# Kernel optimization log

Measured on AMD Instinct MI355X. Metric: run time of the kernel, lower is better.

## Reference

```python
import jax, jax.numpy as jnp
import numpy as np
from jax import lax

B, NUM_E, NUM_R, H, C, K = 8192, 20000, 500, 512, 50, 3
EPS = 1e-5


def batchnorm(x, g, b, axes, shape):
    # training-mode BN: biased batch statistics (matches torch default forward)
    m = jnp.mean(x, axis=axes, keepdims=True)
    v = jnp.var(x, axis=axes, keepdims=True)
    return (x - m) / jnp.sqrt(v + EPS) * g.reshape(shape) + b.reshape(shape)


def setup_inputs() -> dict:
    key = jax.random.key(0)
    ks = jax.random.split(key, 12)
    facts = jax.random.randint(ks[0], (B, 3), 0, NUM_R)
    ent_emb = jax.random.normal(ks[1], (NUM_E, H), jnp.float32)
    rel_emb = jax.random.normal(ks[2], (NUM_R, H), jnp.float32)
    e_r_bias = jax.random.normal(ks[3], (NUM_E, H), jnp.float32)
    conv_w = jax.random.normal(ks[4], (C, 3, K), jnp.float32) * (1.0 / np.sqrt(3 * K))
    conv_b = jnp.zeros((C,), jnp.float32)
    fc_w = jax.random.normal(ks[5], (H, H * C), jnp.float32) * (1.0 / np.sqrt(H * C))
    fc_b = jnp.zeros((H,), jnp.float32)
    bn0_g = jnp.ones((3,), jnp.float32); bn0_b = jnp.zeros((3,), jnp.float32)
    bn1_g = jnp.ones((C,), jnp.float32); bn1_b = jnp.zeros((C,), jnp.float32)
    bn2_g = jnp.ones((H,), jnp.float32); bn2_b = jnp.zeros((H,), jnp.float32)
    return {"facts": facts, "ent_emb": ent_emb, "rel_emb": rel_emb, "e_r_bias": e_r_bias,
            "conv_w": conv_w, "conv_b": conv_b, "fc_w": fc_w, "fc_b": fc_b,
            "bn0_g": bn0_g, "bn0_b": bn0_b, "bn1_g": bn1_g, "bn1_b": bn1_b,
            "bn2_g": bn2_g, "bn2_b": bn2_b}


def reference(facts, ent_emb, rel_emb, e_r_bias, conv_w, conv_b, fc_w, fc_b,
              bn0_g, bn0_b, bn1_g, bn1_b, bn2_g, bn2_b):
    e_s = ent_emb[facts[:, 0]]        # (B, H)
    e_r = rel_emb[facts[:, 1]]        # (B, H)
    bias = e_r_bias[facts[:, 0]]      # (B, H)
    x = jnp.stack([e_s, e_r, bias], axis=1)            # (B, 3, H)
    x = batchnorm(x, bn0_g, bn0_b, (0, 2), (1, 3, 1))  # BatchNorm1d(3)
    pad = K // 2
    x = lax.conv_general_dilated(x, conv_w, window_strides=(1,),
                                 padding=((pad, pad),),
                                 dimension_numbers=("NCH", "OIH", "NCH"))
    x = x + conv_b[None, :, None]                      # (B, C, H)
    x = batchnorm(x, bn1_g, bn1_b, (0, 2), (1, C, 1))  # BatchNorm1d(C)
    x = jax.nn.relu(x)
    x = x.reshape(B, C * H)
    x = x @ fc_w.T + fc_b                              # (B, H)
    x = batchnorm(x, bn2_g, bn2_b, (0,), (1, H))       # BatchNorm1d(H), len>1
    x = jax.nn.relu(x)
    score = x @ ent_emb.T                              # (B, NUM_E)
    # F.softmax then log == log_softmax
    return jax.nn.log_softmax(score, axis=-1)
```

## Files before the change

kernel.cpp:

```cpp
#include <hip/hip_runtime.h>

#define B_SZ   8192
#define NUM_E  20000
#define H_DIM  512
#define C_DIM  50
#define KHW    25600
#define EPS    1e-5f
#define KSPLIT 8

typedef short bf16x8 __attribute__((ext_vector_type(8)));
typedef float f32x4  __attribute__((ext_vector_type(4)));

__device__ __forceinline__ float bf2f(unsigned short u) {
  return __uint_as_float(((unsigned int)u) << 16);
}
__device__ __forceinline__ unsigned short f2bf(float f) {
  unsigned int u = __float_as_uint(f);
  return (unsigned short)((u + 0x7FFFu + ((u >> 16) & 1u)) >> 16);
}

__global__ __launch_bounds__(256) void cvt_bf16_kernel(const float* __restrict__ in,
                                                       unsigned short* __restrict__ out,
                                                       int n4) {
  int i = blockIdx.x * 256 + threadIdx.x;
  int stride = gridDim.x * 256;
  for (; i < n4; i += stride) {
    float4 v = reinterpret_cast<const float4*>(in)[i];
    ushort4 o;
    o.x = f2bf(v.x); o.y = f2bf(v.y); o.z = f2bf(v.z); o.w = f2bf(v.w);
    reinterpret_cast<ushort4*>(out)[i] = o;
  }
}

__global__ __launch_bounds__(256) void bn0_stats_kernel(const int* __restrict__ facts,
                                                        const float* __restrict__ ent,
                                                        const float* __restrict__ rel,
                                                        const float* __restrict__ bias,
                                                        float* __restrict__ stats) {
  const int tid = threadIdx.x;
  float s0=0.f,s1=0.f,s2=0.f,q0=0.f,q1=0.f,q2=0.f;
  const int stride = gridDim.x * 256;
  for (int i = blockIdx.x * 256 + tid; i < B_SZ * H_DIM; i += stride) {
    int b = i >> 9, h = i & 511;
    int f0 = facts[b * 3 + 0], f1 = facts[b * 3 + 1];
    float v0 = ent[f0 * H_DIM + h];
    float v1 = rel[f1 * H_DIM + h];
    float v2 = bias[f0 * H_DIM + h];
    s0 += v0; q0 += v0 * v0;
    s1 += v1; q1 += v1 * v1;
    s2 += v2; q2 += v2 * v2;
  }
  __shared__ float red[256];
  float vals[6] = {s0, s1, s2, q0, q1, q2};
  for (int j = 0; j < 6; ++j) {
    red[tid] = vals[j]; __syncthreads();
    for (int off = 128; off > 0; off >>= 1) {
      if (tid < off) red[tid] += red[tid + off];
      __syncthreads();
    }
    if (tid == 0) atomicAdd(&stats[j], red[0]);
    __syncthreads();
  }
}

__global__ __launch_bounds__(256) void xn_kernel(const int* __restrict__ facts,
                                                 const float* __restrict__ ent,
                                                 const float* __restrict__ rel,
                                                 const float* __restrict__ bias,
                                                 const float* __restrict__ g0,
                                                 const float* __restrict__ b0,
                                                 const float* __restrict__ stats,
                                                 unsigned short* __restrict__ xn) {
  const float invN = 1.0f / 4194304.0f;
  float a[3], c[3];
  #pragma unroll
  for (int ch = 0; ch < 3; ++ch) {
    float mean = stats[ch] * invN;
    float var  = stats[3 + ch] * invN - mean * mean;
    float sc = g0[ch] * rsqrtf(var + EPS);
    a[ch] = sc;
    c[ch] = b0[ch] - mean * sc;
  }
  const int stride = gridDim.x * 256;
  for (int i = blockIdx.x * 256 + threadIdx.x; i < B_SZ * H_DIM; i += stride) {
    int b = i >> 9, h = i & 511;
    int f0 = facts[b * 3 + 0], f1 = facts[b * 3 + 1];
    xn[(b * 3 + 0) * H_DIM + h] = f2bf(fmaf(ent[f0 * H_DIM + h],  a[0], c[0]));
    xn[(b * 3 + 1) * H_DIM + h] = f2bf(fmaf(rel[f1 * H_DIM + h],  a[1], c[1]));
    xn[(b * 3 + 2) * H_DIM + h] = f2bf(fmaf(bias[f0 * H_DIM + h], a[2], c[2]));
  }
}

__global__ __launch_bounds__(256) void conv_stats_kernel(const unsigned short* __restrict__ xn,
                                                         const float* __restrict__ conv_w,
                                                         const float* __restrict__ conv_b,
                                                         float* __restrict__ stats) {
  const int tid = threadIdx.x;
  const int cg = blockIdx.y;
  float w[8][9], cb[8];
  #pragma unroll
  for (int j = 0; j < 8; ++j) {
    int c = cg * 8 + j;
    if (c < C_DIM) {
      #pragma unroll
      for (int t = 0; t < 9; ++t) w[j][t] = conv_w[c * 9 + t];
      cb[j] = conv_b[c];
    } else {
      #pragma unroll
      for (int t = 0; t < 9; ++t) w[j][t] = 0.f;
      cb[j] = 0.f;
    }
  }
  float s[8], qv[8];
  #pragma unroll
  for (int j = 0; j < 8; ++j) { s[j] = 0.f; qv[j] = 0.f; }
  const int stride = gridDim.x * 256;
  for (int i = blockIdx.x * 256 + tid; i < B_SZ * H_DIM; i += stride) {
    int b = i >> 9, h = i & 511;
    float xv[9];
    #pragma unroll
    for (int ii = 0; ii < 3; ++ii) {
      const unsigned short* row = xn + ((size_t)b * 3 + ii) * H_DIM;
      xv[ii * 3 + 0] = (h > 0)   ? bf2f(row[h - 1]) : 0.f;
      xv[ii * 3 + 1] = bf2f(row[h]);
      xv[ii * 3 + 2] = (h < 511) ? bf2f(row[h + 1]) : 0.f;
    }
    #pragma unroll
    for (int j = 0; j < 8; ++j) {
      float v = cb[j];
      #pragma unroll
      for (int t = 0; t < 9; ++t) v = fmaf(w[j][t], xv[t], v);
      s[j] += v; qv[j] += v * v;
    }
  }
  __shared__ float red[256];
  #pragma unroll 1
  for (int j = 0; j < 8; ++j) {
    int c = cg * 8 + j;
    red[tid] = s[j]; __syncthreads();
    for (int off = 128; off > 0; off >>= 1) {
      if (tid < off) red[tid] += red[tid + off];
      __syncthreads();
    }
    if (tid == 0 && c < C_DIM) atomicAdd(&stats[8 + c], red[0]);
    __syncthreads();
    red[tid] = qv[j]; __syncthreads();
    for (int off = 128; off > 0; off >>= 1) {
      if (tid < off) red[tid] += red[tid + off];
      __syncthreads();
    }
    if (tid == 0 && c < C_DIM) atomicAdd(&stats[64 + c], red[0]);
    __syncthreads();
  }
}

__global__ __launch_bounds__(64) void bn1_fold_kernel(const float* __restrict__ conv_w,
                                                      const float* __restrict__ conv_b,
                                                      const float* __restrict__ g1,
                                                      const float* __restrict__ b1,
                                                      const float* __restrict__ stats,
                                                      float* __restrict__ cwf) {
  const int c = threadIdx.x;
  if (c >= C_DIM) return;
  const float invN = 1.0f / 4194304.0f;
  float mean = stats[8 + c] * invN;
  float var  = stats[64 + c] * invN - mean * mean;
  float sc = g1[c] * rsqrtf(var + EPS);
  float tc = fmaf(sc, conv_b[c], b1[c] - mean * sc);
  #pragma unroll
  for (int t = 0; t < 9; ++t) cwf[c * 10 + t] = conv_w[c * 9 + t] * sc;
  cwf[c * 10 + 9] = tc;
}

__global__ __launch_bounds__(256) void fc_gemm_kernel(const unsigned short* __restrict__ xn,
                                                      const unsigned short* __restrict__ fcw,
                                                      const float* __restrict__ cwf,
                                                      float* __restrict__ z) {
  const int tid  = threadIdx.x;
  const int m0   = blockIdx.x * 128;
  const int n0   = blockIdx.y * 128;
  const int hs   = blockIdx.z * 64;
  const int lane = tid & 63;
  const int wave = tid >> 6;
  const int wm   = (wave >> 1) * 64;
  const int wn   = (wave & 1) * 64;
  const int l15  = lane & 15;
  const int qd   = lane >> 4;
  const int am   = tid >> 1;
  const int ah   = (tid & 1) * 16;

  __shared__ unsigned short xstage[128][3][36];
  __shared__ unsigned short albuf[2][128][40];

  f32x4 acc[4][4];
  #pragma unroll
  for (int a = 0; a < 4; ++a)
    #pragma unroll
    for (int b = 0; b < 4; ++b) {
      f32x4 zv = {0.f, 0.f, 0.f, 0.f};
      acc[a][b] = zv;
    }

  const unsigned short* bbase[4];
  #pragma unroll
  for (int tn = 0; tn < 4; ++tn)
    bbase[tn] = fcw + (size_t)(n0 + wn + tn * 16 + l15) * KHW + qd * 8;

  float xw[3][18];

  for (int h0 = hs; h0 < hs + 64; h0 += 32) {
    __syncthreads();
    for (int idx = tid; idx < 128 * 3 * 34; idx += 256) {
      int m = idx / 102;
      int rem = idx - m * 102;
      int i = rem / 34;
      int x = rem - i * 34;
      int h = h0 - 1 + x;
      unsigned short v = 0;
      if (h >= 0 && h < H_DIM) v = xn[((size_t)(m0 + m) * 3 + i) * H_DIM + h];
      xstage[m][i][x] = v;
    }
    __syncthreads();
    #pragma unroll
    for (int i = 0; i < 3; ++i) {
      const unsigned int* p = (const unsigned int*)&xstage[am][i][ah];
      #pragma unroll
      for (int j = 0; j < 9; ++j) {
        unsigned int u = p[j];
        xw[i][2 * j]     = __uint_as_float(u << 16);
        xw[i][2 * j + 1] = __uint_as_float(u & 0xFFFF0000u);
      }
    }

    auto agen = [&](int c, int bb) {
      float w[9], tc;
      const float* cw = cwf + c * 10;
      #pragma unroll
      for (int t = 0; t < 9; ++t) w[t] = cw[t];
      tc = cw[9];
      unsigned int pk[8];
      #pragma unroll
      for (int kp = 0; kp < 8; ++kp) {
        float vv[2];
        #pragma unroll
        for (int e = 0; e < 2; ++e) {
          int kk = kp * 2 + e;
          float v = tc;
          #pragma unroll
          for (int i = 0; i < 3; ++i) {
            v = fmaf(w[i * 3 + 0], xw[i][kk],     v);
            v = fmaf(w[i * 3 + 1], xw[i][kk + 1], v);
            v = fmaf(w[i * 3 + 2], xw[i][kk + 2], v);
          }
          vv[e] = fmaxf(v, 0.f);
        }
        asm("v_cvt_pk_bf16_f32 %0, %1, %2" : "=v"(pk[kp]) : "v"(vv[0]), "v"(vv[1]));
      }
      uint4* d = (uint4*)&albuf[bb][am][ah];
      d[0] = make_uint4(pk[0], pk[1], pk[2], pk[3]);
      d[1] = make_uint4(pk[4], pk[5], pk[6], pk[7]);
    };

    agen(0, 0);
    bf16x8 bcur[4];
    #pragma unroll
    for (int tn = 0; tn < 4; ++tn)
      bcur[tn] = *(const bf16x8*)(bbase[tn] + h0);
    __syncthreads();

    #pragma unroll 1
    for (int c = 0; c < C_DIM; ++c) {
      bf16x8 af[4];
      #pragma unroll
      for (int tm = 0; tm < 4; ++tm)
        af[tm] = *(const bf16x8*)&albuf[c & 1][wm + tm * 16 + l15][qd * 8];
      #pragma unroll
      for (int tm = 0; tm < 4; ++tm)
        #pragma unroll
        for (int tn = 0; tn < 4; ++tn)
          acc[tm][tn] = __builtin_amdgcn_mfma_f32_16x16x32_bf16(af[tm], bcur[tn], acc[tm][tn], 0, 0, 0);
      if (c + 1 < C_DIM) {
        bf16x8 bnew[4];
        #pragma unroll
        for (int tn = 0; tn < 4; ++tn)
          bnew[tn] = *(const bf16x8*)(bbase[tn] + (c + 1) * H_DIM + h0);
        agen(c + 1, (c + 1) & 1);
        __syncthreads();
        #pragma unroll
        for (int tn = 0; tn < 4; ++tn) bcur[tn] = bnew[tn];
      } else {
        __syncthreads();
      }
    }
  }

  #pragma unroll
  for (int tm = 0; tm < 4; ++tm)
    #pragma unroll
    for (int tn = 0; tn < 4; ++tn) {
      int col = n0 + wn + tn * 16 + l15;
      #pragma unroll
      for (int r = 0; r < 4; ++r) {
        int row = m0 + wm + tm * 16 + qd * 4 + r;
        atomicAdd(&z[(size_t)row * H_DIM + col], acc[tm][tn][r]);
      }
    }
}

__global__ __launch_bounds__(256) void bn2_stats_kernel(const float* __restrict__ z,
                                                        float* __restrict__ stats) {
  const int tid = threadIdx.x;
  const int col = blockIdx.y * 64 + (tid & 63);
  float s = 0.f, qq = 0.f;
  for (int r = blockIdx.x * 4 + (tid >> 6); r < B_SZ; r += gridDim.x * 4) {
    float v = z[(size_t)r * H_DIM + col];
    s += v; qq += v * v;
  }
  __shared__ float ls[256], lq[256];
  ls[tid] = s; lq[tid] = qq;
  __syncthreads();
  if (tid < 64) {
    s  = ls[tid] + ls[tid + 64] + ls[tid + 128] + ls[tid + 192];
    qq = lq[tid] + lq[tid + 64] + lq[tid + 128] + lq[tid + 192];
    atomicAdd(&stats[128 + col], s);
    atomicAdd(&stats[640 + col], qq);
  }
}

__global__ __launch_bounds__(256) void zr_kernel(const float* __restrict__ z,
                                                 const float* __restrict__ stats,
                                                 const float* __restrict__ g2,
                                                 const float* __restrict__ b2,
                                                 unsigned short* __restrict__ zrb) {
  const float invB = 1.0f / 8192.0f;
  const int stride = gridDim.x * 256;
  for (int i = blockIdx.x * 256 + threadIdx.x; i < B_SZ * H_DIM; i += stride) {
    int col = i & 511;
    float mean = stats[128 + col] * invB;
    float var  = stats[640 + col] * invB - mean * mean;
    float sc = g2[col] * rsqrtf(var + EPS);
    float tc = b2[col] - mean * sc;
    float v = fmaf(z[i], sc, tc);
    zrb[i] = f2bf(fmaxf(v, 0.f));
  }
}

__global__ __launch_bounds__(256) void score_gemm_kernel(const unsigned short* __restrict__ zrb,
                                                         const unsigned short* __restrict__ entb,
                                                         float* __restrict__ out) {
  const int tid  = threadIdx.x;
  const int m0   = blockIdx.x * 128;
  const int n0   = blockIdx.y * 128;
  const int lane = tid & 63;
  const int wave = tid >> 6;
  const int wm   = (wave >> 1) * 64;
  const int wn   = (wave & 1) * 64;
  const int l15  = lane & 15;
  const int qd   = lane >> 4;

  f32x4 acc[4][4];
  #pragma unroll
  for (int a = 0; a < 4; ++a)
    #pragma unroll
    for (int b = 0; b < 4; ++b) {
      f32x4 zv = {0.f, 0.f, 0.f, 0.f};
      acc[a][b] = zv;
    }

  const unsigned short* ap[4];
  const unsigned short* bp[4];
  #pragma unroll
  for (int t = 0; t < 4; ++t) {
    ap[t] = zrb + (size_t)(m0 + wm + t * 16 + l15) * H_DIM + qd * 8;
    int e = n0 + wn + t * 16 + l15;
    if (e >= NUM_E) e = NUM_E - 1;
    bp[t] = entb + (size_t)e * H_DIM + qd * 8;
  }
  #pragma unroll 2
  for (int k0 = 0; k0 < H_DIM; k0 += 32) {
    bf16x8 af[4], bf[4];
    #pragma unroll
    for (int t = 0; t < 4; ++t) {
      af[t] = *(const bf16x8*)(ap[t] + k0);
      bf[t] = *(const bf16x8*)(bp[t] + k0);
    }
    #pragma unroll
    for (int tm = 0; tm < 4; ++tm)
      #pragma unroll
      for (int tn = 0; tn < 4; ++tn)
        acc[tm][tn] = __builtin_amdgcn_mfma_f32_16x16x32_bf16(af[tm], bf[tn], acc[tm][tn], 0, 0, 0);
  }
  #pragma unroll
  for (int tm = 0; tm < 4; ++tm)
    #pragma unroll
    for (int tn = 0; tn < 4; ++tn) {
      int col = n0 + wn + tn * 16 + l15;
      if (col < NUM_E) {
        #pragma unroll
        for (int r = 0; r < 4; ++r) {
          int row = m0 + wm + tm * 16 + qd * 4 + r;
          out[(size_t)row * NUM_E + col] = acc[tm][tn][r];
        }
      }
    }
}

__global__ __launch_bounds__(256) void logsoftmax_kernel(float* __restrict__ out) {
  const int b = blockIdx.x;
  float* row = out + (size_t)b * NUM_E;
  const int tid = threadIdx.x;
  float m = -3.0e38f, s = 0.f;
  for (int c = tid; c < NUM_E; c += 256) {
    float x = row[c];
    if (x > m) { s = s * __expf(m - x) + 1.f; m = x; }
    else       { s += __expf(x - m); }
  }
  __shared__ float lm[256], ls[256];
  lm[tid] = m; ls[tid] = s;
  __syncthreads();
  for (int off = 128; off > 0; off >>= 1) {
    if (tid < off) {
      float m2 = lm[tid + off], s2 = ls[tid + off];
      float m1 = lm[tid],       s1 = ls[tid];
      float M = fmaxf(m1, m2);
      ls[tid] = s1 * __expf(m1 - M) + s2 * __expf(m2 - M);
      lm[tid] = M;
    }
    __syncthreads();
  }
  const float lse = lm[0] + __logf(ls[0]);
  for (int c = tid; c < NUM_E; c += 256) row[c] -= lse;
}

extern "C" void kernel_launch(void* const* d_in, const int* in_sizes, int n_in,
                              void* d_out, int out_size, void* d_ws, size_t ws_size,
                              hipStream_t stream) {
  const int*   facts  = (const int*)d_in[0];
  const float* ent    = (const float*)d_in[1];
  const float* rel    = (const float*)d_in[2];
  const float* erb    = (const float*)d_in[3];
  const float* conv_w = (const float*)d_in[4];
  const float* conv_b = (const float*)d_in[5];
  const float* fc_w   = (const float*)d_in[6];
  const float* g0     = (const float*)d_in[8];
  const float* b0     = (const float*)d_in[9];
  const float* g1     = (const float*)d_in[10];
  const float* b1     = (const float*)d_in[11];
  const float* g2     = (const float*)d_in[12];
  const float* b2     = (const float*)d_in[13];

  char* ws = (char*)d_ws;
  float*          stats = (float*)ws;
  float*          cwf   = (float*)(ws + 8192);
  unsigned short* xn    = (unsigned short*)(ws + 16384);
  unsigned short* fcw   = (unsigned short*)(ws + 25182208);
  unsigned short* entb  = (unsigned short*)(ws + 51396608);
  float*          z     = (float*)(ws + 71876608);
  unsigned short* zrb   = (unsigned short*)(ws + 88653824);
  float* out = (float*)d_out;

  hipMemsetAsync(stats, 0, 16384, stream);
  hipMemsetAsync(z, 0, 16777216, stream);
  cvt_bf16_kernel<<<2048, 256, 0, stream>>>(ent, entb, (NUM_E * H_DIM) / 4);
  cvt_bf16_kernel<<<2048, 256, 0, stream>>>(fc_w, fcw, (H_DIM * KHW) / 4);
  bn0_stats_kernel<<<1024, 256, 0, stream>>>(facts, ent, rel, erb, stats);
  xn_kernel<<<1024, 256, 0, stream>>>(facts, ent, rel, erb, g0, b0, stats, xn);
  conv_stats_kernel<<<dim3(512, 7), 256, 0, stream>>>(xn, conv_w, conv_b, stats);
  bn1_fold_kernel<<<1, 64, 0, stream>>>(conv_w, conv_b, g1, b1, stats, cwf);
  fc_gemm_kernel<<<dim3(64, 4, KSPLIT), 256, 0, stream>>>(xn, fcw, cwf, z);
  bn2_stats_kernel<<<dim3(64, 8), 256, 0, stream>>>(z, stats);
  zr_kernel<<<2048, 256, 0, stream>>>(z, stats, g2, b2, zrb);
  score_gemm_kernel<<<dim3(64, 157), 256, 0, stream>>>(zrb, entb, out);
  logsoftmax_kernel<<<8192, 256, 0, stream>>>(out);
}
```

Measured before the change: 2.682 ms.

## Fuse partial log-sum-exp into score GEMM and widen FC GEMM tiles to full N

The score GEMM epilogue now computes per-row, per-column-block max and sum-exp partials from its accumulators and writes them to workspace. A small kernel then reduces these into a per-row LSE, and a vectorized kernel subtracts it. This replaces the old logsoftmax pass, which read the output twice. Separately, the FC GEMM now uses 512-thread blocks that each cover all 512 output columns, so the conv-derived A tile is generated once per row block rather than four times, at the cost of more accumulator registers per thread.

```diff
diff --git a/kernel.cpp b/kernel.cpp
--- a/kernel.cpp
+++ b/kernel.cpp
@@ -7,6 +7,7 @@
 #define KHW    25600
 #define EPS    1e-5f
 #define KSPLIT 8
+#define NBLK   157
 
 typedef short bf16x8 __attribute__((ext_vector_type(8)));
 typedef float f32x4  __attribute__((ext_vector_type(4)));
@@ -172,45 +173,44 @@
   cwf[c * 10 + 9] = tc;
 }
 
-__global__ __launch_bounds__(256) void fc_gemm_kernel(const unsigned short* __restrict__ xn,
+__global__ __launch_bounds__(512) void fc_gemm_kernel(const unsigned short* __restrict__ xn,
                                                       const unsigned short* __restrict__ fcw,
                                                       const float* __restrict__ cwf,
                                                       float* __restrict__ z) {
   const int tid  = threadIdx.x;
   const int m0   = blockIdx.x * 128;
-  const int n0   = blockIdx.y * 128;
-  const int hs   = blockIdx.z * 64;
+  const int hs   = blockIdx.y * 64;
   const int lane = tid & 63;
   const int wave = tid >> 6;
-  const int wm   = (wave >> 1) * 64;
-  const int wn   = (wave & 1) * 64;
+  const int wm   = (wave >> 2) * 64;
+  const int wn   = (wave & 3) * 128;
   const int l15  = lane & 15;
   const int qd   = lane >> 4;
-  const int am   = tid >> 1;
-  const int ah   = (tid & 1) * 16;
+  const int am   = tid >> 2;
+  const int ah   = (tid & 3) * 8;
 
   __shared__ unsigned short xstage[128][3][36];
   __shared__ unsigned short albuf[2][128][40];
 
-  f32x4 acc[4][4];
+  f32x4 acc[4][8];
   #pragma unroll
   for (int a = 0; a < 4; ++a)
     #pragma unroll
-    for (int b = 0; b < 4; ++b) {
+    for (int b = 0; b < 8; ++b) {
       f32x4 zv = {0.f, 0.f, 0.f, 0.f};
       acc[a][b] = zv;
     }
 
-  const unsigned short* bbase[4];
-  #pragma unroll
-  for (int tn = 0; tn < 4; ++tn)
-    bbase[tn] = fcw + (size_t)(n0 + wn + tn * 16 + l15) * KHW + qd * 8;
-
-  float xw[3][18];
+  const unsigned short* bbase[8];
+  #pragma unroll
+  for (int tn = 0; tn < 8; ++tn)
+    bbase[tn] = fcw + (size_t)(wn + tn * 16 + l15) * KHW + qd * 8;
+
+  float xw[3][10];
 
   for (int h0 = hs; h0 < hs + 64; h0 += 32) {
     __syncthreads();
-    for (int idx = tid; idx < 128 * 3 * 34; idx += 256) {
+    for (int idx = tid; idx < 128 * 3 * 34; idx += 512) {
       int m = idx / 102;
       int rem = idx - m * 102;
       int i = rem / 34;
@@ -225,7 +225,7 @@
     for (int i = 0; i < 3; ++i) {
       const unsigned int* p = (const unsigned int*)&xstage[am][i][ah];
       #pragma unroll
-      for (int j = 0; j < 9; ++j) {
+      for (int j = 0; j < 5; ++j) {
         unsigned int u = p[j];
         xw[i][2 * j]     = __uint_as_float(u << 16);
         xw[i][2 * j + 1] = __uint_as_float(u & 0xFFFF0000u);
@@ -238,9 +238,9 @@
       #pragma unroll
       for (int t = 0; t < 9; ++t) w[t] = cw[t];
       tc = cw[9];
-      unsigned int pk[8];
-      #pragma unroll
-      for (int kp = 0; kp < 8; ++kp) {
+      unsigned int pk[4];
+      #pragma unroll
+      for (int kp = 0; kp < 4; ++kp) {
         float vv[2];
         #pragma unroll
         for (int e = 0; e < 2; ++e) {
@@ -256,15 +256,13 @@
         }
         asm("v_cvt_pk_bf16_f32 %0, %1, %2" : "=v"(pk[kp]) : "v"(vv[0]), "v"(vv[1]));
       }
-      uint4* d = (uint4*)&albuf[bb][am][ah];
-      d[0] = make_uint4(pk[0], pk[1], pk[2], pk[3]);
-      d[1] = make_uint4(pk[4], pk[5], pk[6], pk[7]);
+      *(uint4*)&albuf[bb][am][ah] = make_uint4(pk[0], pk[1], pk[2], pk[3]);
     };
 
     agen(0, 0);
-    bf16x8 bcur[4];
-    #pragma unroll
-    for (int tn = 0; tn < 4; ++tn)
+    bf16x8 bcur[8];
+    #pragma unroll
+    for (int tn = 0; tn < 8; ++tn)
       bcur[tn] = *(const bf16x8*)(bbase[tn] + h0);
     __syncthreads();
 
@@ -277,17 +275,17 @@
       #pragma unroll
       for (int tm = 0; tm < 4; ++tm)
         #pragma unroll
-        for (int tn = 0; tn < 4; ++tn)
+        for (int tn = 0; tn < 8; ++tn)
           acc[tm][tn] = __builtin_amdgcn_mfma_f32_16x16x32_bf16(af[tm], bcur[tn], acc[tm][tn], 0, 0, 0);
       if (c + 1 < C_DIM) {
-        bf16x8 bnew[4];
+        bf16x8 bnew[8];
         #pragma unroll
-        for (int tn = 0; tn < 4; ++tn)
+        for (int tn = 0; tn < 8; ++tn)
           bnew[tn] = *(const bf16x8*)(bbase[tn] + (c + 1) * H_DIM + h0);
         agen(c + 1, (c + 1) & 1);
         __syncthreads();
         #pragma unroll
-        for (int tn = 0; tn < 4; ++tn) bcur[tn] = bnew[tn];
+        for (int tn = 0; tn < 8; ++tn) bcur[tn] = bnew[tn];
       } else {
         __syncthreads();
       }
@@ -297,8 +295,8 @@
   #pragma unroll
   for (int tm = 0; tm < 4; ++tm)
     #pragma unroll
-    for (int tn = 0; tn < 4; ++tn) {
-      int col = n0 + wn + tn * 16 + l15;
+    for (int tn = 0; tn < 8; ++tn) {
+      int col = wn + tn * 16 + l15;
       #pragma unroll
       for (int r = 0; r < 4; ++r) {
         int row = m0 + wm + tm * 16 + qd * 4 + r;
@@ -347,7 +345,9 @@
 
 __global__ __launch_bounds__(256) void score_gemm_kernel(const unsigned short* __restrict__ zrb,
                                                          const unsigned short* __restrict__ entb,
-                                                         float* __restrict__ out) {
+                                                         float* __restrict__ out,
+                                                         float* __restrict__ pm,
+                                                         float* __restrict__ ps) {
   const int tid  = threadIdx.x;
   const int m0   = blockIdx.x * 128;
   const int n0   = blockIdx.y * 128;
@@ -403,33 +403,77 @@
         }
       }
     }
-}
-
-__global__ __launch_bounds__(256) void logsoftmax_kernel(float* __restrict__ out) {
-  const int b = blockIdx.x;
-  float* row = out + (size_t)b * NUM_E;
-  const int tid = threadIdx.x;
-  float m = -3.0e38f, s = 0.f;
-  for (int c = tid; c < NUM_E; c += 256) {
-    float x = row[c];
-    if (x > m) { s = s * __expf(m - x) + 1.f; m = x; }
-    else       { s += __expf(x - m); }
-  }
-  __shared__ float lm[256], ls[256];
-  lm[tid] = m; ls[tid] = s;
+
+  __shared__ float smx[2][2][4][4][4];
+  __shared__ float ssx[2][2][4][4][4];
+  const int wmb = wave >> 1, wnb = wave & 1;
+  #pragma unroll
+  for (int tm = 0; tm < 4; ++tm) {
+    #pragma unroll
+    for (int r = 0; r < 4; ++r) {
+      float m = -3.0e38f;
+      #pragma unroll
+      for (int tn = 0; tn < 4; ++tn) {
+        int col = n0 + wn + tn * 16 + l15;
+        if (col < NUM_E) m = fmaxf(m, acc[tm][tn][r]);
+      }
+      float s = 0.f;
+      #pragma unroll
+      for (int tn = 0; tn < 4; ++tn) {
+        int col = n0 + wn + tn * 16 + l15;
+        if (col < NUM_E) s += __expf(acc[tm][tn][r] - m);
+      }
+      #pragma unroll
+      for (int d = 1; d < 16; d <<= 1) {
+        float m2 = __shfl_xor(m, d, 64);
+        float s2 = __shfl_xor(s, d, 64);
+        float Mn = fmaxf(m, m2);
+        s = s * __expf(m - Mn) + s2 * __expf(m2 - Mn);
+        m = Mn;
+      }
+      if (l15 == 0) { smx[wmb][wnb][tm][qd][r] = m; ssx[wmb][wnb][tm][qd][r] = s; }
+    }
+  }
   __syncthreads();
-  for (int off = 128; off > 0; off >>= 1) {
-    if (tid < off) {
-      float m2 = lm[tid + off], s2 = ls[tid + off];
-      float m1 = lm[tid],       s1 = ls[tid];
-      float M = fmaxf(m1, m2);
-      ls[tid] = s1 * __expf(m1 - M) + s2 * __expf(m2 - M);
-      lm[tid] = M;
-    }
-    __syncthreads();
-  }
-  const float lse = lm[0] + __logf(ls[0]);
-  for (int c = tid; c < NUM_E; c += 256) row[c] -= lse;
+  if (tid < 128) {
+    int wmb2 = tid >> 6, rl = tid & 63;
+    int tm = rl >> 4, qd2 = (rl >> 2) & 3, r = rl & 3;
+    float m1 = smx[wmb2][0][tm][qd2][r], s1 = ssx[wmb2][0][tm][qd2][r];
+    float m2 = smx[wmb2][1][tm][qd2][r], s2 = ssx[wmb2][1][tm][qd2][r];
+    float Mn = fmaxf(m1, m2);
+    float S  = s1 * __expf(m1 - Mn) + s2 * __expf(m2 - Mn);
+    int row  = m0 + wmb2 * 64 + rl;
+    pm[(size_t)blockIdx.y * B_SZ + row] = Mn;
+    ps[(size_t)blockIdx.y * B_SZ + row] = S;
+  }
+}
+
+__global__ __launch_bounds__(256) void lse_reduce_kernel(const float* __restrict__ pm,
+                                                         const float* __restrict__ ps,
+                                                         float* __restrict__ lse) {
+  int row = blockIdx.x * 256 + threadIdx.x;
+  float M = -3.0e38f, S = 0.f;
+  for (int nb = 0; nb < NBLK; ++nb) {
+    float m2 = pm[(size_t)nb * B_SZ + row];
+    float s2 = ps[(size_t)nb * B_SZ + row];
+    float Mn = fmaxf(M, m2);
+    S = S * __expf(M - Mn) + s2 * __expf(m2 - Mn);
+    M = Mn;
+  }
+  lse[row] = M + __logf(S);
+}
+
+__global__ __launch_bounds__(256) void lsub_kernel(float* __restrict__ out,
+                                                   const float* __restrict__ lse) {
+  const int row = blockIdx.y;
+  const float l = lse[row];
+  float4* p = (float4*)(out + (size_t)row * NUM_E);
+  int i = blockIdx.x * 256 + threadIdx.x;
+  if (i < NUM_E / 4) {
+    float4 v = p[i];
+    v.x -= l; v.y -= l; v.z -= l; v.w -= l;
+    p[i] = v;
+  }
 }
 
 extern "C" void kernel_launch(void* const* d_in, const int* in_sizes, int n_in,
@@ -457,6 +501,9 @@
   unsigned short* entb  = (unsigned short*)(ws + 51396608);
   float*          z     = (float*)(ws + 71876608);
   unsigned short* zrb   = (unsigned short*)(ws + 88653824);
+  float*          pm    = (float*)(ws + 71876608);
+  float*          psx   = (float*)(ws + 71876608 + 5144576);
+  float*          lse   = (float*)(ws + 71876608 + 10289152);
   float* out = (float*)d_out;
 
   hipMemsetAsync(stats, 0, 16384, stream);
@@ -467,9 +514,10 @@
   xn_kernel<<<1024, 256, 0, stream>>>(facts, ent, rel, erb, g0, b0, stats, xn);
   conv_stats_kernel<<<dim3(512, 7), 256, 0, stream>>>(xn, conv_w, conv_b, stats);
   bn1_fold_kernel<<<1, 64, 0, stream>>>(conv_w, conv_b, g1, b1, stats, cwf);
-  fc_gemm_kernel<<<dim3(64, 4, KSPLIT), 256, 0, stream>>>(xn, fcw, cwf, z);
+  fc_gemm_kernel<<<dim3(64, KSPLIT), 512, 0, stream>>>(xn, fcw, cwf, z);
   bn2_stats_kernel<<<dim3(64, 8), 256, 0, stream>>>(z, stats);
   zr_kernel<<<2048, 256, 0, stream>>>(z, stats, g2, b2, zrb);
-  score_gemm_kernel<<<dim3(64, 157), 256, 0, stream>>>(zrb, entb, out);
-  logsoftmax_kernel<<<8192, 256, 0, stream>>>(out);
-}
+  score_gemm_kernel<<<dim3(64, NBLK), 256, 0, stream>>>(zrb, entb, out, pm, psx);
+  lse_reduce_kernel<<<32, 256, 0, stream>>>(pm, psx, lse);
+  lsub_kernel<<<dim3(20, 8192), 256, 0, stream>>>(out, lse);
+}
```

New measurement: 2.526 ms. -5.8%, faster.
